# Optimization experiments

Measured on AMD Instinct MI355X. Metric: run time of the kernel, lower is better.

The kernel has to match this reference:

```python
import jax, jax.numpy as jnp
import numpy as np

B, S, D, L = 16, 512, 256, 8192
DROP_P = 0.2


def setup_inputs() -> dict:
    key = jax.random.key(0)
    k1, k2, k3 = jax.random.split(key, 3)
    x = jax.random.normal(k1, (B, S, D), dtype=jnp.float32)
    label_emb = jax.random.normal(k2, (B, L, D), dtype=jnp.float32)
    mask = jax.random.uniform(k3, (B, S)) < 0.9
    return {"x": x, "mask": mask, "label_emb": label_emb}


def reference(x, mask, label_emb):
    # scores = x @ label_emb^T : [B, S, L]
    scores = jnp.einsum("bsd,bld->bsl", x, label_emb)
    # softmax over label dim (last)
    probs = jax.nn.softmax(scores, axis=-1)
    # post-softmax token masking (non-standard order, faithful to original)
    probs = jnp.where(mask[:, :, None], probs, jnp.zeros((), probs.dtype))
    # dropout (training=True in original), deterministic key for reproducibility
    keep = jax.random.bernoulli(jax.random.key(42), 1.0 - DROP_P, probs.shape)
    probs = jnp.where(keep, probs / (1.0 - DROP_P), jnp.zeros((), probs.dtype))
    # attention pooling: scores^T @ x : [B, L, D]
    return jnp.einsum("bsl,bsd->bld", probs, x)
```

## Files before the change

### kernel.cpp

```cpp
#include <hip/hip_runtime.h>
#include <stdint.h>
#include <stddef.h>

#define B_ 16
#define S_ 512
#define D_ 256
#define L_ 8192

typedef unsigned short u16;
typedef _Float16 f16;
typedef f16 f16x4 __attribute__((ext_vector_type(4)));
typedef f16 f16x8 __attribute__((ext_vector_type(8)));
typedef float f32x4 __attribute__((ext_vector_type(4)));

__device__ __forceinline__ void gl16(const void* g, void* l) {
  __builtin_amdgcn_global_load_lds(
      (const __attribute__((address_space(1))) unsigned int*)g,
      (__attribute__((address_space(3))) unsigned int*)l, 16, 0, 0);
}

__device__ __forceinline__ uint32_t rotl32(uint32_t x, int r) {
  return (x << r) | (x >> (32 - r));
}
__device__ __forceinline__ bool drop_keep(uint32_t j) {
  const uint32_t k0 = 0u, k1 = 42u, k2 = 0x1BD11BDAu ^ k0 ^ k1;
  uint32_t v0 = 0u + k0;
  uint32_t v1 = j + k1;
#define TF_R(r) { v0 += v1; v1 = rotl32(v1, (r)); v1 ^= v0; }
  TF_R(13) TF_R(15) TF_R(26) TF_R(6)
  v0 += k1; v1 += k2 + 1u;
  TF_R(17) TF_R(29) TF_R(16) TF_R(24)
  v0 += k2; v1 += k0 + 2u;
  TF_R(13) TF_R(15) TF_R(26) TF_R(6)
  v0 += k0; v1 += k1 + 3u;
  TF_R(17) TF_R(29) TF_R(16) TF_R(24)
  v0 += k1; v1 += k2 + 4u;
  TF_R(13) TF_R(15) TF_R(26) TF_R(6)
  v0 += k2; v1 += k0 + 5u;
#undef TF_R
  uint32_t bits = v0 ^ v1;
  float u = __uint_as_float((bits >> 9) | 0x3f800000u) - 1.0f;
  return u < 0.8f;
}

__global__ __launch_bounds__(256)
void conv16_kernel(const float* __restrict__ src, f16* __restrict__ dst, int n) {
  int i = (blockIdx.x * 256 + threadIdx.x) * 8;
  if (i >= n) return;
  float4 a = *(const float4*)&src[i];
  float4 b = *(const float4*)&src[i + 4];
  f16x8 o;
  o[0] = (f16)a.x; o[1] = (f16)a.y; o[2] = (f16)a.z; o[3] = (f16)a.w;
  o[4] = (f16)b.x; o[5] = (f16)b.y; o[6] = (f16)b.z; o[7] = (f16)b.w;
  *(f16x8*)&dst[i] = o;
}

__global__ __launch_bounds__(256)
void xt16_kernel(const float* __restrict__ x, f16* __restrict__ xT) {
  const int b = blockIdx.z, sb = blockIdx.x * 32, db = blockIdx.y * 32;
  __shared__ float t[32][33];
  const int tid = threadIdx.x;
  const int r = tid >> 3, c4 = (tid & 7) * 4;
  float4 v = *(const float4*)&x[((size_t)b * S_ + sb + r) * D_ + db + c4];
  t[r][c4] = v.x; t[r][c4 + 1] = v.y; t[r][c4 + 2] = v.z; t[r][c4 + 3] = v.w;
  __syncthreads();
  const int dr = tid >> 3, s4 = (tid & 7) * 4;
  f16x4 o;
#pragma unroll
  for (int j = 0; j < 4; ++j) o[j] = (f16)t[s4 + j][dr];
  *(f16x4*)&xT[((size_t)b * D_ + db + dr) * S_ + sb + s4] = o;
}

__global__ __launch_bounds__(256)
void gemm1t_f16(const f16* __restrict__ eh, const f16* __restrict__ xh,
                float* __restrict__ scoresT, float2* __restrict__ partials) {
  __shared__ __align__(16) f16 As[2][4096];
  __shared__ __align__(16) f16 Bs[2][4096];
  __shared__ float pmaxA[128][2];
  __shared__ float psumA[128][2];

  const int tid = threadIdx.x;
  const int lane = tid & 63, wave = tid >> 6;
  const int b = blockIdx.z, lt = blockIdx.x * 128, st = blockIdx.y * 128;

  const int lm = lane & 15, kq = lane >> 4;
  const int wm = (wave & 1) * 64, wn = (wave >> 1) * 64;
  const int ca = (wave & 1) * 4, cb = (wave >> 1) * 4;

  const int srow = lane & 15, sko = (lane >> 4) * 8;
  auto stage = [&](int bi, int k0) {
#pragma unroll
    for (int i = 0; i < 2; ++i) {
      const int c = wave * 2 + i;
      gl16(eh + ((size_t)b * L_ + lt + c * 16 + srow) * D_ + k0 + sko,
           (char*)As[bi] + c * 1024 + lane * 16);
      gl16(xh + ((size_t)b * S_ + st + c * 16 + srow) * D_ + k0 + sko,
           (char*)Bs[bi] + c * 1024 + lane * 16);
    }
  };

  f32x4 acc[4][4] = {};

  stage(0, 0);
  __syncthreads();
  int bi = 0;
  for (int t = 0; t < 8; ++t) {
    if (t < 7) stage(bi ^ 1, (t + 1) * 32);
    f16x8 fa[4], fb[4];
#pragma unroll
    for (int mi = 0; mi < 4; ++mi)
      fa[mi] = *(const f16x8*)&As[bi][((ca + mi) * 64 + kq * 16 + lm) * 8];
#pragma unroll
    for (int ni = 0; ni < 4; ++ni)
      fb[ni] = *(const f16x8*)&Bs[bi][((cb + ni) * 64 + kq * 16 + lm) * 8];
#pragma unroll
    for (int mi = 0; mi < 4; ++mi)
#pragma unroll
      for (int ni = 0; ni < 4; ++ni)
        acc[mi][ni] = __builtin_amdgcn_mfma_f32_16x16x32_f16(
            fa[mi], fb[ni], acc[mi][ni], 0, 0, 0);
    __syncthreads();
    bi ^= 1;
  }

#pragma unroll
  for (int mi = 0; mi < 4; ++mi)
#pragma unroll
    for (int ni = 0; ni < 4; ++ni) {
      const int l0 = wm + mi * 16 + kq * 4;
      const int s = wn + ni * 16 + lm;
      float* sp = scoresT + ((size_t)b * L_ + lt + l0) * S_ + st + s;
#pragma unroll
      for (int r = 0; r < 4; ++r) sp[(size_t)r * S_] = acc[mi][ni][r];
    }

  float cmax[4];
#pragma unroll
  for (int ni = 0; ni < 4; ++ni) {
    float v = acc[0][ni][0];
#pragma unroll
    for (int mi = 0; mi < 4; ++mi)
#pragma unroll
      for (int r = 0; r < 4; ++r) v = fmaxf(v, acc[mi][ni][r]);
    cmax[ni] = v;
  }
#pragma unroll
  for (int ni = 0; ni < 4; ++ni) {
    cmax[ni] = fmaxf(cmax[ni], __shfl_xor(cmax[ni], 16, 64));
    cmax[ni] = fmaxf(cmax[ni], __shfl_xor(cmax[ni], 32, 64));
  }
  if (kq == 0) {
#pragma unroll
    for (int ni = 0; ni < 4; ++ni) pmaxA[wn + ni * 16 + lm][wave & 1] = cmax[ni];
  }
  __syncthreads();
  float colm[4];
#pragma unroll
  for (int ni = 0; ni < 4; ++ni) {
    const int s = wn + ni * 16 + lm;
    colm[ni] = fmaxf(pmaxA[s][0], pmaxA[s][1]);
  }
  float psum[4] = {};
#pragma unroll
  for (int ni = 0; ni < 4; ++ni)
#pragma unroll
    for (int mi = 0; mi < 4; ++mi)
#pragma unroll
      for (int r = 0; r < 4; ++r)
        psum[ni] += __expf(acc[mi][ni][r] - colm[ni]);
#pragma unroll
  for (int ni = 0; ni < 4; ++ni) {
    psum[ni] += __shfl_xor(psum[ni], 16, 64);
    psum[ni] += __shfl_xor(psum[ni], 32, 64);
  }
  if (kq == 0) {
#pragma unroll
    for (int ni = 0; ni < 4; ++ni) psumA[wn + ni * 16 + lm][wave & 1] = psum[ni];
  }
  __syncthreads();
  if (tid < 128) {
    float m = fmaxf(pmaxA[tid][0], pmaxA[tid][1]);
    float Z = psumA[tid][0] + psumA[tid][1];
    partials[((size_t)b * 64 + blockIdx.x) * S_ + st + tid] = make_float2(m, Z);
  }
}

__global__ __launch_bounds__(256)
void combine_kernel(const float2* __restrict__ partials,
                    const int* __restrict__ mask, float2* __restrict__ stats) {
  const int idx = blockIdx.x * 256 + threadIdx.x;
  const int b = idx / S_, si = idx - b * S_;
  float m = -3.402823466e38f, Z = 0.f;
  for (int t = 0; t < 64; ++t) {
    float2 p = partials[((size_t)b * 64 + t) * S_ + si];
    if (p.x > m) {
      Z = Z * __expf(m - p.x) + p.y;
      m = p.x;
    } else {
      Z += p.y * __expf(p.x - m);
    }
  }
  float f = (mask[idx] != 0) ? (1.25f / Z) : 0.0f;
  stats[idx] = make_float2(m, f);
}

__global__ __launch_bounds__(512)
void gemm2_fused(const float* __restrict__ scoresT, const f16* __restrict__ xT,
                 const float2* __restrict__ stats, float* __restrict__ out) {
  __shared__ __align__(16) f16 Bs[2][8192];
  __shared__ float2 stat_s[S_];

  const int tid = threadIdx.x;
  const int lane = tid & 63, wave = tid >> 6;
  const int b = blockIdx.z, lt = blockIdx.x * 128;

  stat_s[tid] = stats[b * S_ + tid];

  const int lm = lane & 15, kq = lane >> 4;
  const int l_loc = wave * 16 + lm;
  const uint32_t gbase =
      (uint32_t)(b * S_) * (uint32_t)L_ + (uint32_t)(lt + l_loc);

  const int srow = lane & 15, sko = (lane >> 4) * 8;
  const size_t xb_base = (size_t)b * D_ * S_;
  auto stage = [&](int bi, int k0) {
#pragma unroll
    for (int i = 0; i < 2; ++i) {
      const int c = wave * 2 + i;
      gl16(xT + xb_base + (size_t)(c * 16 + srow) * S_ + k0 + sko,
           (char*)Bs[bi] + c * 1024 + lane * 16);
    }
  };

  const float* srowp =
      scoresT + ((size_t)b * L_ + lt + l_loc) * S_ + kq * 8;

  f32x4 acc[16] = {};

  f32x4 sv0 = *(const f32x4*)&srowp[0];
  f32x4 sv1 = *(const f32x4*)&srowp[4];
  stage(0, 0);
  __syncthreads();
  int bi = 0;
  for (int k0 = 0; k0 < S_; k0 += 32) {
    f32x4 nv0, nv1;
    const bool more = (k0 < S_ - 32);
    if (more) {
      stage(bi ^ 1, k0 + 32);
      nv0 = *(const f32x4*)&srowp[k0 + 32];
      nv1 = *(const f32x4*)&srowp[k0 + 36];
    }

    float pv[8];
#pragma unroll
    for (int j = 0; j < 4; ++j) {
      const float2 mf = stat_s[k0 + kq * 8 + j];
      pv[j] = __expf(sv0[j] - mf.x) * mf.y;
    }
#pragma unroll
    for (int j = 0; j < 4; ++j) {
      const float2 mf = stat_s[k0 + kq * 8 + 4 + j];
      pv[4 + j] = __expf(sv1[j] - mf.x) * mf.y;
    }
    f16x8 fa;
#pragma unroll
    for (int j = 0; j < 8; ++j) {
      const uint32_t gidx = gbase + (uint32_t)(k0 + kq * 8 + j) * (uint32_t)L_;
      fa[j] = drop_keep(gidx) ? (f16)pv[j] : (f16)0.f;
    }

#pragma unroll
    for (int ni = 0; ni < 16; ++ni) {
      const f16x8 fb = *(const f16x8*)&Bs[bi][(ni * 64 + kq * 16 + lm) * 8];
      acc[ni] = __builtin_amdgcn_mfma_f32_16x16x32_f16(fa, fb, acc[ni], 0, 0, 0);
    }
    __syncthreads();
    if (more) { sv0 = nv0; sv1 = nv1; }
    bi ^= 1;
  }

#pragma unroll
  for (int ni = 0; ni < 16; ++ni) {
    const int n = ni * 16 + lm;
    float* op = out + ((size_t)b * L_ + lt + wave * 16 + kq * 4) * D_ + n;
#pragma unroll
    for (int r = 0; r < 4; ++r) op[(size_t)r * D_] = acc[ni][r];
  }
}

extern "C" void kernel_launch(void* const* d_in, const int* in_sizes, int n_in,
                              void* d_out, int out_size, void* d_ws, size_t ws_size,
                              hipStream_t stream) {
  const float* x = (const float*)d_in[0];
  const int* mask = (const int*)d_in[1];
  const float* E = (const float*)d_in[2];
  float* out = (float*)d_out;

  char* ws = (char*)d_ws;
  const size_t nE = (size_t)B_ * L_ * D_;
  const size_t nX = (size_t)B_ * S_ * D_;
  size_t o = 0;
  f16* Eh = (f16*)(ws + o); o += nE * 2;
  f16* Xh = (f16*)(ws + o); o += nX * 2;
  f16* XT = (f16*)(ws + o); o += nX * 2;
  float2* stats = (float2*)(ws + o); o += (size_t)B_ * S_ * 8;
  float2* partials = (float2*)(ws + o); o += (size_t)B_ * 64 * S_ * 8;
  float* scoresT = (float*)(ws + o);

  conv16_kernel<<<dim3((unsigned)(nE / 8 / 256)), 256, 0, stream>>>(E, Eh, (int)nE);
  conv16_kernel<<<dim3((unsigned)(nX / 8 / 256)), 256, 0, stream>>>(x, Xh, (int)nX);
  xt16_kernel<<<dim3(S_ / 32, D_ / 32, B_), 256, 0, stream>>>(x, XT);

  gemm1t_f16<<<dim3(L_ / 128, S_ / 128, B_), 256, 0, stream>>>(
      Eh, Xh, scoresT, partials);
  combine_kernel<<<dim3(B_ * S_ / 256), 256, 0, stream>>>(partials, mask, stats);
  gemm2_fused<<<dim3(L_ / 128, 1, B_), 512, 0, stream>>>(scoresT, XT, stats, out);
}
```

Measured before the change: 571.7 us.

## Precompute dropout keep-bits in gemm1 and pass bitmask to gemm2

Moves the hash-based dropout keep computation out of gemm2's inner loop and into gemm1, where it is interleaved with the MFMA main loop. The bits are packed into 32-bit words in a new workspace buffer, and gemm2 reads one uint4 per thread and selects values with bit tests. The intent is to hide the integer hashing under gemm1's matrix work and lighten gemm2's per-step ALU load. The cost is extra integer work and register use in gemm1, plus an extra global write and read of the bitmask (about 8 MB).

```diff
diff --git a/kernel.cpp b/kernel.cpp
--- a/kernel.cpp
+++ b/kernel.cpp
@@ -73,7 +73,8 @@
 
 __global__ __launch_bounds__(256)
 void gemm1t_f16(const f16* __restrict__ eh, const f16* __restrict__ xh,
-                float* __restrict__ scoresT, float2* __restrict__ partials) {
+                float* __restrict__ scoresT, float2* __restrict__ partials,
+                uint32_t* __restrict__ kb) {
   __shared__ __align__(16) f16 As[2][4096];
   __shared__ __align__(16) f16 Bs[2][4096];
   __shared__ float pmaxA[128][2];
@@ -99,6 +100,10 @@
     }
   };
 
+  const int q0 = (tid & 1) * 2;
+  const int ml = lt + (tid >> 1);
+  uint32_t wlo = 0, whi = 0;
+
   f32x4 acc[4][4] = {};
 
   stage(0, 0);
@@ -106,6 +111,20 @@
   int bi = 0;
   for (int t = 0; t < 8; ++t) {
     if (t < 7) stage(bi ^ 1, (t + 1) * 32);
+
+    {
+      const int c = t & 3, q = q0 + (t >> 2);
+      const uint32_t base =
+          (uint32_t)(b * S_ + st + 32 * c + 8 * q) * (uint32_t)L_ +
+          (uint32_t)ml;
+      uint32_t byte = 0;
+#pragma unroll
+      for (int j = 0; j < 8; ++j)
+        byte |= (uint32_t)drop_keep(base + (uint32_t)j * L_) << j;
+      if (t < 4) wlo |= byte << (8 * c);
+      else       whi |= byte << (8 * c);
+    }
+
     f16x8 fa[4], fb[4];
 #pragma unroll
     for (int mi = 0; mi < 4; ++mi)
@@ -121,6 +140,12 @@
             fa[mi], fb[ni], acc[mi][ni], 0, 0, 0);
     __syncthreads();
     bi ^= 1;
+  }
+
+  {
+    uint32_t* kp = kb + ((size_t)b * L_ + ml) * 16 + blockIdx.y;
+    kp[q0 * 4] = wlo;
+    kp[(q0 + 1) * 4] = whi;
   }
 
 #pragma unroll
@@ -206,7 +231,8 @@
 
 __global__ __launch_bounds__(512)
 void gemm2_fused(const float* __restrict__ scoresT, const f16* __restrict__ xT,
-                 const float2* __restrict__ stats, float* __restrict__ out) {
+                 const float2* __restrict__ stats,
+                 const uint32_t* __restrict__ kb, float* __restrict__ out) {
   __shared__ __align__(16) f16 Bs[2][8192];
   __shared__ float2 stat_s[S_];
 
@@ -218,8 +244,6 @@
 
   const int lm = lane & 15, kq = lane >> 4;
   const int l_loc = wave * 16 + lm;
-  const uint32_t gbase =
-      (uint32_t)(b * S_) * (uint32_t)L_ + (uint32_t)(lt + l_loc);
 
   const int srow = lane & 15, sko = (lane >> 4) * 8;
   const size_t xb_base = (size_t)b * D_ * S_;
@@ -235,48 +259,55 @@
   const float* srowp =
       scoresT + ((size_t)b * L_ + lt + l_loc) * S_ + kq * 8;
 
+  const uint4 kwv = *(const uint4*)(kb + ((size_t)b * L_ + lt + l_loc) * 16 +
+                                    kq * 4);
+  const uint32_t kwa[4] = {kwv.x, kwv.y, kwv.z, kwv.w};
+
   f32x4 acc[16] = {};
 
   f32x4 sv0 = *(const f32x4*)&srowp[0];
   f32x4 sv1 = *(const f32x4*)&srowp[4];
   stage(0, 0);
   __syncthreads();
-  int bi = 0;
-  for (int k0 = 0; k0 < S_; k0 += 32) {
-    f32x4 nv0, nv1;
-    const bool more = (k0 < S_ - 32);
-    if (more) {
-      stage(bi ^ 1, k0 + 32);
-      nv0 = *(const f32x4*)&srowp[k0 + 32];
-      nv1 = *(const f32x4*)&srowp[k0 + 36];
-    }
-
-    float pv[8];
-#pragma unroll
-    for (int j = 0; j < 4; ++j) {
-      const float2 mf = stat_s[k0 + kq * 8 + j];
-      pv[j] = __expf(sv0[j] - mf.x) * mf.y;
-    }
-#pragma unroll
-    for (int j = 0; j < 4; ++j) {
-      const float2 mf = stat_s[k0 + kq * 8 + 4 + j];
-      pv[4 + j] = __expf(sv1[j] - mf.x) * mf.y;
-    }
-    f16x8 fa;
-#pragma unroll
-    for (int j = 0; j < 8; ++j) {
-      const uint32_t gidx = gbase + (uint32_t)(k0 + kq * 8 + j) * (uint32_t)L_;
-      fa[j] = drop_keep(gidx) ? (f16)pv[j] : (f16)0.f;
-    }
-
-#pragma unroll
-    for (int ni = 0; ni < 16; ++ni) {
-      const f16x8 fb = *(const f16x8*)&Bs[bi][(ni * 64 + kq * 16 + lm) * 8];
-      acc[ni] = __builtin_amdgcn_mfma_f32_16x16x32_f16(fa, fb, acc[ni], 0, 0, 0);
-    }
-    __syncthreads();
-    if (more) { sv0 = nv0; sv1 = nv1; }
-    bi ^= 1;
+#pragma unroll
+  for (int kg = 0; kg < 4; ++kg) {
+#pragma unroll
+    for (int c = 0; c < 4; ++c) {
+      const int kk = kg * 4 + c;
+      const int k0 = kk * 32;
+      const int bi = kk & 1;
+      f32x4 nv0, nv1;
+      if (kk < 15) {
+        stage(bi ^ 1, k0 + 32);
+        nv0 = *(const f32x4*)&srowp[k0 + 32];
+        nv1 = *(const f32x4*)&srowp[k0 + 36];
+      }
+
+      float pv[8];
+#pragma unroll
+      for (int j = 0; j < 4; ++j) {
+        const float2 mf = stat_s[k0 + kq * 8 + j];
+        pv[j] = __expf(sv0[j] - mf.x) * mf.y;
+      }
+#pragma unroll
+      for (int j = 0; j < 4; ++j) {
+        const float2 mf = stat_s[k0 + kq * 8 + 4 + j];
+        pv[4 + j] = __expf(sv1[j] - mf.x) * mf.y;
+      }
+      const uint32_t mbyte = (kwa[kg] >> (c * 8)) & 0xffu;
+      f16x8 fa;
+#pragma unroll
+      for (int j = 0; j < 8; ++j)
+        fa[j] = ((mbyte >> j) & 1u) ? (f16)pv[j] : (f16)0.f;
+
+#pragma unroll
+      for (int ni = 0; ni < 16; ++ni) {
+        const f16x8 fb = *(const f16x8*)&Bs[bi][(ni * 64 + kq * 16 + lm) * 8];
+        acc[ni] = __builtin_amdgcn_mfma_f32_16x16x32_f16(fa, fb, acc[ni], 0, 0, 0);
+      }
+      __syncthreads();
+      if (kk < 15) { sv0 = nv0; sv1 = nv1; }
+    }
   }
 
 #pragma unroll
@@ -305,6 +336,7 @@
   f16* XT = (f16*)(ws + o); o += nX * 2;
   float2* stats = (float2*)(ws + o); o += (size_t)B_ * S_ * 8;
   float2* partials = (float2*)(ws + o); o += (size_t)B_ * 64 * S_ * 8;
+  uint32_t* kb = (uint32_t*)(ws + o); o += (size_t)B_ * L_ * 16 * 4;
   float* scoresT = (float*)(ws + o);
 
   conv16_kernel<<<dim3((unsigned)(nE / 8 / 256)), 256, 0, stream>>>(E, Eh, (int)nE);
@@ -312,7 +344,7 @@
   xt16_kernel<<<dim3(S_ / 32, D_ / 32, B_), 256, 0, stream>>>(x, XT);
 
   gemm1t_f16<<<dim3(L_ / 128, S_ / 128, B_), 256, 0, stream>>>(
-      Eh, Xh, scoresT, partials);
+      Eh, Xh, scoresT, partials, kb);
   combine_kernel<<<dim3(B_ * S_ / 256), 256, 0, stream>>>(partials, mask, stats);
-  gemm2_fused<<<dim3(L_ / 128, 1, B_), 512, 0, stream>>>(scoresT, XT, stats, out);
-}
+  gemm2_fused<<<dim3(L_ / 128, 1, B_), 512, 0, stream>>>(scoresT, XT, stats, kb, out);
+}
```

New measurement: 523.7 us. 1.09x faster.
